# Kernel tuning notes

Hardware: AMD Instinct MI355X
Metric: run time of the kernel (lower is better)

Reference implementation:

```python
import jax, jax.numpy as jnp
import numpy as np

L, B, T, D, H = 8, 4, 1024, 1024, 16
DH = D // H
TPB, NB = 16, 64  # tokens_per_block, max_blocks; T == TPB*NB
EPS = 1e-5


def _block_causal_mask():
    idx = jnp.arange(T)
    causal = idx[:, None] >= idx[None, :]
    blk = idx // TPB
    block_diag = blk[:, None] == blk[None, :]
    return causal | block_diag  # [T, T] bool


def _ln(x, g, b):
    mu = jnp.mean(x, axis=-1, keepdims=True)
    var = jnp.mean(jnp.square(x - mu), axis=-1, keepdims=True)
    return (x - mu) * jax.lax.rsqrt(var + EPS) * g + b


def setup_inputs() -> dict:
    key = jax.random.key(0)
    ks = jax.random.split(key, 8)
    s = 0.02
    inp = {
        'sequences': jax.random.normal(ks[0], (B, T, D), jnp.float32),
        'Wq': jax.random.normal(ks[1], (L, D, D), jnp.float32) * s,
        'bq': jnp.zeros((L, D), jnp.float32),
        'Wk': jax.random.normal(ks[2], (L, D, D), jnp.float32) * s,
        'bk': jnp.zeros((L, D), jnp.float32),
        'Wv': jax.random.normal(ks[3], (L, D, D), jnp.float32) * s,
        'bv': jnp.zeros((L, D), jnp.float32),
        'Wp': jax.random.normal(ks[4], (L, D, D), jnp.float32) * s,
        'bp': jnp.zeros((L, D), jnp.float32),
        'ln1_g': jnp.ones((L, D), jnp.float32),
        'ln1_b': jnp.zeros((L, D), jnp.float32),
        'ln2_g': jnp.ones((L, D), jnp.float32),
        'ln2_b': jnp.zeros((L, D), jnp.float32),
        'W1': jax.random.normal(ks[5], (L, D, 4 * D), jnp.float32) * s,
        'b1': jnp.zeros((L, 4 * D), jnp.float32),
        'W2': jax.random.normal(ks[6], (L, 4 * D, D), jnp.float32) * s,
        'b2': jnp.zeros((L, D), jnp.float32),
        'lnf_g': jnp.ones((D,), jnp.float32),
        'lnf_b': jnp.zeros((D,), jnp.float32),
    }
    return inp


def reference(sequences, Wq, bq, Wk, bk, Wv, bv, Wp, bp,
              ln1_g, ln1_b, ln2_g, ln2_b, W1, b1, W2, b2, lnf_g, lnf_b):
    mask = _block_causal_mask()
    scale = 1.0 / np.sqrt(DH)
    x = sequences
    for i in range(L):
        h = _ln(x, ln1_g[i], ln1_b[i])
        q = (h @ Wq[i] + bq[i]).reshape(B, T, H, DH)
        k = (h @ Wk[i] + bk[i]).reshape(B, T, H, DH)
        v = (h @ Wv[i] + bv[i]).reshape(B, T, H, DH)
        att = jnp.einsum('bthd,bshd->bhts', q, k) * scale  # [B,H,T,T]
        att = jnp.where(mask, att, -jnp.inf)
        att = jax.nn.softmax(att, axis=-1)
        y = jnp.einsum('bhts,bshd->bthd', att, v).reshape(B, T, D)
        x = x + (y @ Wp[i] + bp[i])
        h2 = _ln(x, ln2_g[i], ln2_b[i])
        ff = jax.nn.gelu(h2 @ W1[i] + b1[i], approximate=False) @ W2[i] + b2[i]
        x = x + ff
    return _ln(x, lnf_g, lnf_b)
```

## Files before the change

kernel.cpp:

```cpp
#include <hip/hip_runtime.h>
#include <hip/hip_bf16.h>
#include <math.h>

#define B_ 4
#define T_ 1024
#define D_ 1024
#define H_ 16
#define DH_ 64
#define M_ 4096
#define QSTR_ 3072
#define EPS_ 1e-5f

typedef __attribute__((ext_vector_type(4))) float f32x4;
typedef __attribute__((ext_vector_type(8))) short s16x8;

#if __has_builtin(__builtin_amdgcn_exp2f)
#define EXP2F __builtin_amdgcn_exp2f
#else
#define EXP2F exp2f
#endif

__device__ __forceinline__ float gelu_f(float x) {
  return 0.5f * x * (1.0f + erff(x * 0.70710678118654752f));
}
__device__ __forceinline__ float b2f(unsigned short u) {
  union { unsigned int i; float f; } c; c.i = ((unsigned int)u) << 16; return c.f;
}
__device__ __forceinline__ unsigned short f2b(float f) {
  __hip_bfloat16 h = __float2bfloat16(f);
  return *reinterpret_cast<unsigned short*>(&h);
}
__device__ __forceinline__ void g2l16(void* l, const void* g) {
  __builtin_amdgcn_global_load_lds(
      (const __attribute__((address_space(1))) void*)g,
      (__attribute__((address_space(3))) void*)l, 16, 0, 0);
}

template<bool BF16OUT>
__global__ __launch_bounds__(256) void ln_kernel(
    const float* __restrict__ in, void* __restrict__ out,
    const float* __restrict__ g, const float* __restrict__ b) {
  const int row = blockIdx.x;
  const int tid = threadIdx.x;
  const float* rp = in + (size_t)row * D_;
  float4 v = *reinterpret_cast<const float4*>(rp + tid * 4);
  float s = v.x + v.y + v.z + v.w;
  float s2 = v.x * v.x + v.y * v.y + v.z * v.z + v.w * v.w;
#pragma unroll
  for (int off = 1; off < 64; off <<= 1) {
    s += __shfl_xor(s, off);
    s2 += __shfl_xor(s2, off);
  }
  __shared__ float red[2][4];
  const int wid = tid >> 6;
  if ((tid & 63) == 0) { red[0][wid] = s; red[1][wid] = s2; }
  __syncthreads();
  s = red[0][0] + red[0][1] + red[0][2] + red[0][3];
  s2 = red[1][0] + red[1][1] + red[1][2] + red[1][3];
  const float mu = s * (1.0f / D_);
  const float var = s2 * (1.0f / D_) - mu * mu;
  const float rs = rsqrtf(var + EPS_);
  float4 gv = *reinterpret_cast<const float4*>(g + tid * 4);
  float4 bv = *reinterpret_cast<const float4*>(b + tid * 4);
  float o0 = (v.x - mu) * rs * gv.x + bv.x;
  float o1 = (v.y - mu) * rs * gv.y + bv.y;
  float o2 = (v.z - mu) * rs * gv.z + bv.z;
  float o3 = (v.w - mu) * rs * gv.w + bv.w;
  if (BF16OUT) {
    ushort4 pk;
    pk.x = f2b(o0); pk.y = f2b(o1); pk.z = f2b(o2); pk.w = f2b(o3);
    *reinterpret_cast<ushort4*>((unsigned short*)out + (size_t)row * D_ + tid * 4) = pk;
  } else {
    *reinterpret_cast<float4*>((float*)out + (size_t)row * D_ + tid * 4) =
        make_float4(o0, o1, o2, o3);
  }
}

__global__ __launch_bounds__(256) void concat_bias(
    const float* __restrict__ bq, const float* __restrict__ bk,
    const float* __restrict__ bv, float* __restrict__ out) {
  const int i = blockIdx.x * 256 + threadIdx.x;
  const int l = i / QSTR_, c = i % QSTR_;
  const float* src = (c < 1024) ? bq : ((c < 2048) ? bk : bv);
  out[i] = src[l * 1024 + (c & 1023)];
}

__global__ __launch_bounds__(256) void reduce_add(
    float* __restrict__ x, const float* __restrict__ p) {
  const int i = blockIdx.x * 256 + threadIdx.x;
  float4 a = reinterpret_cast<float4*>(x)[i];
  float4 b = reinterpret_cast<const float4*>(p)[i];
  a.x += b.x; a.y += b.y; a.z += b.z; a.w += b.w;
  reinterpret_cast<float4*>(x)[i] = a;
}

__device__ __forceinline__ void transpose_tile(
    const float* __restrict__ src, int sld,
    __hip_bfloat16* __restrict__ dst, int dld, int k0, int n0) {
  __shared__ float tile[32][33];
  const int t = threadIdx.x;
  const int r = t >> 3;
  const int cq = (t & 7) * 4;
  float4 vv = *reinterpret_cast<const float4*>(src + (size_t)(k0 + r) * sld + n0 + cq);
  tile[r][cq + 0] = vv.x; tile[r][cq + 1] = vv.y;
  tile[r][cq + 2] = vv.z; tile[r][cq + 3] = vv.w;
  __syncthreads();
  ushort4 o;
  o.x = f2b(tile[cq + 0][r]); o.y = f2b(tile[cq + 1][r]);
  o.z = f2b(tile[cq + 2][r]); o.w = f2b(tile[cq + 3][r]);
  *reinterpret_cast<ushort4*>((unsigned short*)dst + (size_t)(n0 + r) * dld + k0 + cq) = o;
}

struct TrAll {
  const float *wq, *wk, *wv, *wp, *w1, *w2;
  __hip_bfloat16 *dqkv, *dp, *d1, *d2;
};

__global__ __launch_bounds__(256) void transpose_all(TrAll a) {
  const int t = blockIdx.x;
  const float* src;
  __hip_bfloat16* dst;
  int sld, dld, k0, n0;
  if (t < 4096) {
    const int m = t >> 10, tile = t & 1023;
    k0 = (tile >> 5) * 32; n0 = (tile & 31) * 32;
    src = (m == 0) ? a.wq : (m == 1) ? a.wk : (m == 2) ? a.wv : a.wp;
    sld = 1024; dld = 1024;
    dst = (m < 3) ? (a.dqkv + (size_t)m * 1024 * 1024) : a.dp;
  } else if (t < 8192) {
    const int tile = t - 4096;
    k0 = (tile & 31) * 32; n0 = (tile >> 5) * 32;
    src = a.w1; sld = 4096; dst = a.d1; dld = 1024;
  } else {
    const int tile = t - 8192;
    k0 = (tile >> 5) * 32; n0 = (tile & 31) * 32;
    src = a.w2; sld = 1024; dst = a.d2; dld = 4096;
  }
  transpose_tile(src, sld, dst, dld, k0, n0);
}

template<int MODE, int BN>
__global__ __launch_bounds__(256) void gemm_mfma(
    const __hip_bfloat16* __restrict__ A,
    const __hip_bfloat16* __restrict__ Bt,
    const float* __restrict__ bias,
    void* __restrict__ Cout, int N, int K) {
  __shared__ short As[3][128 * 32];
  __shared__ short Bs[3][BN * 32];
  int bid = blockIdx.y * gridDim.x + blockIdx.x;
  const int nwg = gridDim.x * gridDim.y;
  bid = (bid & 7) * (nwg >> 3) + (bid >> 3);
  const int gn = (bid % gridDim.x) * BN;
  const int gm = (bid / gridDim.x) * 128;

  const int tid = threadIdx.x;
  const int wid = tid >> 6, lane = tid & 63;
  constexpr int MR = (BN == 128) ? 4 : 2;
  const int wm = (BN == 128) ? (wid >> 1) : wid;
  const int wn = (BN == 128) ? (wid & 1) : 0;
  const int fr = lane & 15, kg = lane >> 4;

  const int ldr = lane >> 2;
  const int ldk = (((lane & 3) ^ ((lane >> 3) & 3)) * 8);
  const unsigned short* ap =
      (const unsigned short*)A + (size_t)(gm + wid * 32 + ldr) * K + ldk;
  const unsigned short* bp =
      (const unsigned short*)Bt +
      (size_t)(gn + ((BN == 128) ? wid * 32 : wid * 16) + ldr) * K + ldk;

  const int nkt = K >> 5;

#define STAGE_T(t, buf)                                                    \
  {                                                                        \
    const unsigned short* a_ = ap + (size_t)(t) * 32;                      \
    g2l16((char*)As[buf] + (wid * 2) * 1024, a_);                          \
    g2l16((char*)As[buf] + (wid * 2 + 1) * 1024, a_ + (size_t)16 * K);     \
    const unsigned short* b_ = bp + (size_t)(t) * 32;                      \
    if (BN == 128) {                                                       \
      g2l16((char*)Bs[buf] + (wid * 2) * 1024, b_);                        \
      g2l16((char*)Bs[buf] + (wid * 2 + 1) * 1024, b_ + (size_t)16 * K);   \
    } else {                                                               \
      g2l16((char*)Bs[buf] + wid * 1024, b_);                              \
    }                                                                      \
  }

  STAGE_T(0, 0);
  STAGE_T(1, 1);

  const int cxa = (kg ^ ((fr >> 1) & 3)) * 8;
  f32x4 acc[MR][4] = {};
  for (int t = 0; t < nkt; ++t) {
    const int buf = t % 3;
    if (t + 2 < nkt) STAGE_T(t + 2, (t + 2) % 3);
    const int rem = nkt - 1 - t;
    if (rem >= 2) {
      if (BN == 128) asm volatile("s_waitcnt vmcnt(8)" ::: "memory");
      else           asm volatile("s_waitcnt vmcnt(6)" ::: "memory");
    } else if (rem == 1) {
      if (BN == 128) asm volatile("s_waitcnt vmcnt(4)" ::: "memory");
      else           asm volatile("s_waitcnt vmcnt(3)" ::: "memory");
    } else {
      asm volatile("s_waitcnt vmcnt(0)" ::: "memory");
    }
    __builtin_amdgcn_s_barrier();
    __builtin_amdgcn_sched_barrier(0);
    s16x8 af[MR], bfr[4];
#pragma unroll
    for (int m = 0; m < MR; ++m)
      af[m] = *reinterpret_cast<const s16x8*>(
          &As[buf][(wm * (16 * MR) + m * 16 + fr) * 32 + cxa]);
#pragma unroll
    for (int n = 0; n < 4; ++n)
      bfr[n] = *reinterpret_cast<const s16x8*>(
          &Bs[buf][(wn * 64 + n * 16 + fr) * 32 + cxa]);
#pragma unroll
    for (int m = 0; m < MR; ++m)
#pragma unroll
      for (int n = 0; n < 4; ++n)
        acc[m][n] = __builtin_amdgcn_mfma_f32_16x16x32_bf16(af[m], bfr[n], acc[m][n], 0, 0, 0);
    __builtin_amdgcn_sched_barrier(0);
    __builtin_amdgcn_s_barrier();
  }
#undef STAGE_T

  const int r0 = gm + wm * (16 * MR);
  const int c0 = gn + wn * 64;
  float bb[4];
#pragma unroll
  for (int n = 0; n < 4; ++n)
    bb[n] = bias ? bias[c0 + n * 16 + fr] : 0.0f;
#pragma unroll
  for (int m = 0; m < MR; ++m) {
#pragma unroll
    for (int j = 0; j < 4; ++j) {
      const int row = r0 + m * 16 + kg * 4 + j;
#pragma unroll
      for (int n = 0; n < 4; ++n) {
        float val = acc[m][n][j] + bb[n];
        const size_t idx = (size_t)row * N + c0 + n * 16 + fr;
        if (MODE == 0) {
          ((unsigned short*)Cout)[idx] = f2b(val);
        } else if (MODE == 1) {
          float* cp = (float*)Cout + idx;
          *cp = *cp + val;
        } else {
          ((unsigned short*)Cout)[idx] = f2b(gelu_f(val));
        }
      }
    }
  }
}

template<int MODE>
__global__ __launch_bounds__(512) void gemm_w256(
    const __hip_bfloat16* __restrict__ A,
    const __hip_bfloat16* __restrict__ Bt,
    const float* __restrict__ bias,
    void* __restrict__ Cout, float* __restrict__ P,
    int N, int K, int KS) {
  __shared__ short As[3][128 * 32];
  __shared__ short Bs[3][256 * 32];
  int bid = blockIdx.y * gridDim.x + blockIdx.x;
  const int nwg = gridDim.x * gridDim.y;
  bid = (bid & 7) * (nwg >> 3) + (bid >> 3);
  const int gn = (bid % gridDim.x) * 256;
  const int gm = (bid / gridDim.x) * 128;
  const int koff = (MODE == 3) ? blockIdx.z * KS : 0;

  const int tid = threadIdx.x;
  const int wid = tid >> 6, lane = tid & 63;
  const int wm = wid & 1, wn = wid >> 1;
  const int fr = lane & 15, kg = lane >> 4;

  const int ldr = lane >> 2;
  const int ldk = (((lane & 3) ^ ((lane >> 3) & 3)) * 8);
  const unsigned short* ap =
      (const unsigned short*)A + (size_t)(gm + wid * 16 + ldr) * K + koff + ldk;
  const unsigned short* bp =
      (const unsigned short*)Bt + (size_t)(gn + wid * 32 + ldr) * K + koff + ldk;

  const int nkt = ((MODE == 3) ? KS : K) >> 5;

#define STAGE_W(t, buf)                                                    \
  {                                                                        \
    g2l16((char*)As[buf] + wid * 1024, ap + (size_t)(t) * 32);             \
    const unsigned short* b_ = bp + (size_t)(t) * 32;                      \
    g2l16((char*)Bs[buf] + (wid * 2) * 1024, b_);                          \
    g2l16((char*)Bs[buf] + (wid * 2 + 1) * 1024, b_ + (size_t)16 * K);     \
  }

  STAGE_W(0, 0);
  STAGE_W(1, 1);

  const int cxa = (kg ^ ((fr >> 1) & 3)) * 8;
  f32x4 acc[4][4] = {};
  for (int t = 0; t < nkt; ++t) {
    const int buf = t % 3;
    if (t + 2 < nkt) STAGE_W(t + 2, (t + 2) % 3);
    const int rem = nkt - 1 - t;
    if (rem >= 2)      asm volatile("s_waitcnt vmcnt(6)" ::: "memory");
    else if (rem == 1) asm volatile("s_waitcnt vmcnt(3)" ::: "memory");
    else               asm volatile("s_waitcnt vmcnt(0)" ::: "memory");
    __builtin_amdgcn_s_barrier();
    __builtin_amdgcn_sched_barrier(0);
    s16x8 af[4], bfr[4];
#pragma unroll
    for (int m = 0; m < 4; ++m)
      af[m] = *reinterpret_cast<const s16x8*>(
          &As[buf][(wm * 64 + m * 16 + fr) * 32 + cxa]);
#pragma unroll
    for (int n = 0; n < 4; ++n)
      bfr[n] = *reinterpret_cast<const s16x8*>(
          &Bs[buf][(wn * 64 + n * 16 + fr) * 32 + cxa]);
#pragma unroll
    for (int m = 0; m < 4; ++m)
#pragma unroll
      for (int n = 0; n < 4; ++n)
        acc[m][n] = __builtin_amdgcn_mfma_f32_16x16x32_bf16(af[m], bfr[n], acc[m][n], 0, 0, 0);
    __builtin_amdgcn_sched_barrier(0);
    __builtin_amdgcn_s_barrier();
  }
#undef STAGE_W

  const int r0 = gm + wm * 64;
  const int c0 = gn + wn * 64;
  if (MODE == 3 && blockIdx.z == 1) {
#pragma unroll
    for (int m = 0; m < 4; ++m)
#pragma unroll
      for (int j = 0; j < 4; ++j) {
        const int row = r0 + m * 16 + kg * 4 + j;
#pragma unroll
        for (int n = 0; n < 4; ++n)
          P[(size_t)row * N + c0 + n * 16 + fr] = acc[m][n][j];
      }
    return;
  }
  float bb[4];
#pragma unroll
  for (int n = 0; n < 4; ++n)
    bb[n] = bias ? bias[c0 + n * 16 + fr] : 0.0f;
#pragma unroll
  for (int m = 0; m < 4; ++m) {
#pragma unroll
    for (int j = 0; j < 4; ++j) {
      const int row = r0 + m * 16 + kg * 4 + j;
#pragma unroll
      for (int n = 0; n < 4; ++n) {
        float val = acc[m][n][j] + bb[n];
        const size_t idx = (size_t)row * N + c0 + n * 16 + fr;
        if (MODE == 0) {
          ((unsigned short*)Cout)[idx] = f2b(val);
        } else if (MODE == 1 || MODE == 3) {
          float* cp = (float*)Cout + idx;
          *cp = *cp + val;
        } else {
          ((unsigned short*)Cout)[idx] = f2b(gelu_f(val));
        }
      }
    }
  }
}

__global__ __launch_bounds__(256) void attn_mfma(
    const __hip_bfloat16* __restrict__ qkv, __hip_bfloat16* __restrict__ yg) {
  const int qb = 7 - blockIdx.x;
  const int hh = blockIdx.y;
  const int bb = blockIdx.z;
  __shared__ short Qs[128 * 64];
  __shared__ short Ks[64 * 64];
  __shared__ short Vt[64 * 64];
  const int tid = threadIdx.x;
  const int wid = tid >> 6, lane = tid & 63;
  const int fr = lane & 15, kg = lane >> 4;
  const size_t qb_base = (size_t)bb * T_ * QSTR_ + (size_t)hh * DH_;
  const unsigned short* qgp = (const unsigned short*)qkv + qb_base;
  const unsigned short* kgp = qgp + 1024;
  const unsigned short* vgp = qgp + 2048;
  const float C = 0.125f * 1.4426950408889634f;

  {
    const int r8 = lane >> 3, cp = lane & 7;
#pragma unroll
    for (int u = 0; u < 4; ++u) {
      const int row = wid * 32 + u * 8 + r8;
      const int c16 = cp ^ (row & 7);
      g2l16((char*)Qs + (wid * 32 + u * 8) * 128,
            qgp + (size_t)(qb * 128 + row) * QSTR_ + c16 * 8);
    }
  }
  asm volatile("s_waitcnt vmcnt(0)" ::: "memory");
  __syncthreads();
  s16x8 qf[2][2];
#pragma unroll
  for (int rg = 0; rg < 2; ++rg) {
    const int row = wid * 32 + rg * 16 + fr;
    const char* rp = (const char*)Qs + row * 128;
    qf[rg][0] = *reinterpret_cast<const s16x8*>(rp + (((0 + kg) ^ (row & 7)) << 4));
    qf[rg][1] = *reinterpret_cast<const s16x8*>(rp + (((4 + kg) ^ (row & 7)) << 4));
  }

  f32x4 acco[2][4] = {};
  float m_run[2][4], l_run[2][4];
#pragma unroll
  for (int rg = 0; rg < 2; ++rg)
#pragma unroll
    for (int j = 0; j < 4; ++j) { m_run[rg][j] = -INFINITY; l_run[rg][j] = 0.f; }

  const int q16hi = qb * 8 + wid * 2 + 1;
  const int ntile = 2 * qb + 2;
  for (int kt = 0; kt < ntile; ++kt) {
    __syncthreads();
    {
      const int r8 = lane >> 3, cp = lane & 7;
#pragma unroll
      for (int u = 0; u < 2; ++u) {
        const int row = wid * 16 + u * 8 + r8;
        const int c16 = cp ^ (row & 7);
        g2l16((char*)Ks + (wid * 16 + u * 8) * 128,
              kgp + (size_t)(kt * 64 + row) * QSTR_ + c16 * 8);
      }
    }
    {
      const int kv0 = tid >> 3;
      const int d0 = (tid & 7) * 8;
      const int rot = tid & 7;
#pragma unroll
      for (int u = 0; u < 2; ++u) {
        const int kv = u * 32 + kv0;
        s16x8 sv = *reinterpret_cast<const s16x8*>(
            vgp + (size_t)(kt * 64 + kv) * QSTR_ + d0);
#pragma unroll
        for (int j = 0; j < 8; ++j) {
          const int jj = (j + rot) & 7;
          const int d = d0 + jj;
          *(short*)((char*)Vt + d * 128 + ((((kv >> 3) ^ jj) & 7) << 4) + (kv & 7) * 2) = sv[jj];
        }
      }
    }
    asm volatile("s_waitcnt vmcnt(0)" ::: "memory");
    __syncthreads();

    if (kt * 4 <= q16hi) {
      f32x4 accs[2][4] = {};
#pragma unroll
      for (int n = 0; n < 4; ++n) {
        const int row = n * 16 + fr;
        const char* rp = (const char*)Ks + row * 128;
        s16x8 kf0 = *reinterpret_cast<const s16x8*>(rp + (((0 + kg) ^ (row & 7)) << 4));
        s16x8 kf1 = *reinterpret_cast<const s16x8*>(rp + (((4 + kg) ^ (row & 7)) << 4));
#pragma unroll
        for (int rg = 0; rg < 2; ++rg) {
          accs[rg][n] = __builtin_amdgcn_mfma_f32_16x16x32_bf16(qf[rg][0], kf0, accs[rg][n], 0, 0, 0);
          accs[rg][n] = __builtin_amdgcn_mfma_f32_16x16x32_bf16(qf[rg][1], kf1, accs[rg][n], 0, 0, 0);
        }
      }
#pragma unroll
      for (int rg = 0; rg < 2; ++rg) {
        const int q16 = qb * 8 + wid * 2 + rg;
        float mloc[4] = {-3.0e38f, -3.0e38f, -3.0e38f, -3.0e38f};
#pragma unroll
        for (int n = 0; n < 4; ++n)
          if (kt * 4 + n <= q16)
#pragma unroll
            for (int j = 0; j < 4; ++j) mloc[j] = fmaxf(mloc[j], accs[rg][n][j]);
#pragma unroll
        for (int off = 1; off < 16; off <<= 1)
#pragma unroll
          for (int j = 0; j < 4; ++j) mloc[j] = fmaxf(mloc[j], __shfl_xor(mloc[j], off));
        float a_[4];
#pragma unroll
        for (int j = 0; j < 4; ++j) {
          const float mn = fmaxf(m_run[rg][j], mloc[j]);
          a_[j] = EXP2F((m_run[rg][j] - mn) * C);
          m_run[rg][j] = mn;
        }
        float psum[4] = {};
#pragma unroll
        for (int n = 0; n < 4; ++n) {
          const bool dead = (kt * 4 + n > q16);
          const int c16b = n * 2 + (fr >> 3);
#pragma unroll
          for (int j = 0; j < 4; ++j) {
            float p = dead ? 0.0f : EXP2F((accs[rg][n][j] - m_run[rg][j]) * C);
            psum[j] += p;
            const int row = wid * 32 + rg * 16 + kg * 4 + j;
            *(short*)((char*)Qs + row * 128 + (((c16b ^ (row & 7)) & 7) << 4) + (fr & 7) * 2) =
                (short)f2b(p);
          }
        }
#pragma unroll
        for (int j = 0; j < 4; ++j) l_run[rg][j] = l_run[rg][j] * a_[j] + psum[j];
#pragma unroll
        for (int dt = 0; dt < 4; ++dt)
#pragma unroll
          for (int j = 0; j < 4; ++j) acco[rg][dt][j] *= a_[j];
      }
#pragma unroll
      for (int rg = 0; rg < 2; ++rg) {
        const int prow = wid * 32 + rg * 16 + fr;
        const char* pp = (const char*)Qs + prow * 128;
#pragma unroll
        for (int kk = 0; kk < 2; ++kk) {
          const s16x8 pf = *reinterpret_cast<const s16x8*>(
              pp + ((((kk * 4 + kg) ^ (prow & 7)) & 7) << 4));
#pragma unroll
          for (int dt = 0; dt < 4; ++dt) {
            const int vrow = dt * 16 + fr;
            const s16x8 vf = *reinterpret_cast<const s16x8*>(
                (const char*)Vt + vrow * 128 + ((((kk * 4 + kg) ^ (vrow & 7)) & 7) << 4));
            acco[rg][dt] = __builtin_amdgcn_mfma_f32_16x16x32_bf16(pf, vf, acco[rg][dt], 0, 0, 0);
          }
        }
      }
    }
  }

#pragma unroll
  for (int off = 1; off < 16; off <<= 1)
#pragma unroll
    for (int rg = 0; rg < 2; ++rg)
#pragma unroll
      for (int j = 0; j < 4; ++j) l_run[rg][j] += __shfl_xor(l_run[rg][j], off);
  unsigned short* yp = (unsigned short*)yg + (size_t)bb * T_ * D_ + (size_t)hh * DH_;
#pragma unroll
  for (int rg = 0; rg < 2; ++rg) {
    float inv[4];
#pragma unroll
    for (int j = 0; j < 4; ++j) inv[j] = 1.0f / l_run[rg][j];
#pragma unroll
    for (int dt = 0; dt < 4; ++dt)
#pragma unroll
      for (int j = 0; j < 4; ++j) {
        const int row = qb * 128 + wid * 32 + rg * 16 + kg * 4 + j;
        yp[(size_t)row * D_ + dt * 16 + fr] = f2b(acco[rg][dt][j] * inv[j]);
      }
  }
}

extern "C" void kernel_launch(void* const* d_in, const int* in_sizes, int n_in,
                              void* d_out, int out_size, void* d_ws, size_t ws_size,
                              hipStream_t stream) {
  (void)in_sizes; (void)n_in; (void)out_size; (void)ws_size;
  const float* seq  = (const float*)d_in[0];
  const float* Wq   = (const float*)d_in[1];
  const float* bq   = (const float*)d_in[2];
  const float* Wk   = (const float*)d_in[3];
  const float* bk   = (const float*)d_in[4];
  const float* Wv   = (const float*)d_in[5];
  const float* bv   = (const float*)d_in[6];
  const float* Wp   = (const float*)d_in[7];
  const float* bp   = (const float*)d_in[8];
  const float* ln1g = (const float*)d_in[9];
  const float* ln1b = (const float*)d_in[10];
  const float* ln2g = (const float*)d_in[11];
  const float* ln2b = (const float*)d_in[12];
  const float* W1   = (const float*)d_in[13];
  const float* b1   = (const float*)d_in[14];
  const float* W2   = (const float*)d_in[15];
  const float* b2   = (const float*)d_in[16];
  const float* lnfg = (const float*)d_in[17];
  const float* lnfb = (const float*)d_in[18];

  float* x = (float*)d_out;
  char* ws = (char*)d_ws;
  const size_t MB = 1024ull * 1024ull;
  typedef __hip_bfloat16 bf16;
  bf16*  wtqkv = (bf16*)(ws + 0 * MB);
  bf16*  wtp   = (bf16*)(ws + 6 * MB);
  bf16*  wtF1  = (bf16*)(ws + 8 * MB);
  bf16*  wtF2  = (bf16*)(ws + 16 * MB);
  bf16*  hb    = (bf16*)(ws + 24 * MB);
  bf16*  qkv   = (bf16*)(ws + 32 * MB);
  bf16*  mid   = (bf16*)(ws + 56 * MB);
  float* bqkv  = (float*)(ws + 88 * MB);
  float* part  = (float*)(ws + 32 * MB);

  hipMemcpyAsync(x, seq, (size_t)M_ * D_ * sizeof(float), hipMemcpyDeviceToDevice, stream);

  const dim3 blk(256);
  const dim3 blkw(512);
  concat_bias<<<96, blk, 0, stream>>>(bq, bk, bv, bqkv);

  for (int i = 0; i < 8; ++i) {
    const size_t wo  = (size_t)i * D_ * D_;
    const size_t vo  = (size_t)i * D_;
    const size_t w1o = (size_t)i * D_ * 4 * D_;

    ln_kernel<true><<<M_, blk, 0, stream>>>(x, hb, ln1g + vo, ln1b + vo);
    TrAll ta;
    ta.wq = Wq + wo; ta.wk = Wk + wo; ta.wv = Wv + wo; ta.wp = Wp + wo;
    ta.w1 = W1 + w1o; ta.w2 = W2 + w1o;
    ta.dqkv = wtqkv; ta.dp = wtp; ta.d1 = wtF1; ta.d2 = wtF2;
    transpose_all<<<12288, blk, 0, stream>>>(ta);
    gemm_w256<0><<<dim3(12, 32), blkw, 0, stream>>>(
        hb, wtqkv, bqkv + (size_t)i * QSTR_, qkv, nullptr, QSTR_, 1024, 0);
    attn_mfma<<<dim3(8, 16, 4), blk, 0, stream>>>(qkv, hb);
    gemm_mfma<1, 64><<<dim3(16, 32), blk, 0, stream>>>(hb, wtp, bp + vo, x, 1024, 1024);
    ln_kernel<true><<<M_, blk, 0, stream>>>(x, hb, ln2g + vo, ln2b + vo);
    gemm_w256<2><<<dim3(16, 32), blkw, 0, stream>>>(
        hb, wtF1, b1 + (size_t)i * 4096, mid, nullptr, 4096, 1024, 0);
    gemm_w256<3><<<dim3(4, 32, 2), blkw, 0, stream>>>(
        mid, wtF2, b2 + vo, x, part, 1024, 4096, 2048);
    reduce_add<<<4096, blk, 0, stream>>>(x, part);
  }
  ln_kernel<false><<<M_, blk, 0, stream>>>(x, x, lnfg, lnfb);
}
```

Measured before the change: 2.171 ms.

## Fuse split-K residual add into layernorm and double-buffer K/V in attention

Removes the separate reduce_add kernel. The split-K partial sum from the FFN2 GEMM is now added to x inside the next layer's LN1 kernel, or the final LN, which also writes the updated residual back. The attention kernel now double-buffers the K and V^T tiles in LDS, prefetching the next tile's K via global_load_lds and V into registers while the current tile is computed. The goal is to save one launch and a full pass over memory per layer, and to hide global load latency in attention, at the cost of more LDS and registers per block.

```diff
diff --git a/kernel.cpp b/kernel.cpp
--- a/kernel.cpp
+++ b/kernel.cpp
@@ -36,14 +36,20 @@
       (__attribute__((address_space(3))) void*)l, 16, 0, 0);
 }
 
-template<bool BF16OUT>
+template<bool BF16OUT, bool ADDP>
 __global__ __launch_bounds__(256) void ln_kernel(
-    const float* __restrict__ in, void* __restrict__ out,
+    float* __restrict__ xio, const float* __restrict__ part,
+    void* __restrict__ out,
     const float* __restrict__ g, const float* __restrict__ b) {
   const int row = blockIdx.x;
   const int tid = threadIdx.x;
-  const float* rp = in + (size_t)row * D_;
+  float* rp = xio + (size_t)row * D_;
   float4 v = *reinterpret_cast<const float4*>(rp + tid * 4);
+  if (ADDP) {
+    float4 pv = *reinterpret_cast<const float4*>(part + (size_t)row * D_ + tid * 4);
+    v.x += pv.x; v.y += pv.y; v.z += pv.z; v.w += pv.w;
+    *reinterpret_cast<float4*>(rp + tid * 4) = v;
+  }
   float s = v.x + v.y + v.z + v.w;
   float s2 = v.x * v.x + v.y * v.y + v.z * v.z + v.w * v.w;
 #pragma unroll
@@ -85,15 +91,6 @@
   out[i] = src[l * 1024 + (c & 1023)];
 }
 
-__global__ __launch_bounds__(256) void reduce_add(
-    float* __restrict__ x, const float* __restrict__ p) {
-  const int i = blockIdx.x * 256 + threadIdx.x;
-  float4 a = reinterpret_cast<float4*>(x)[i];
-  float4 b = reinterpret_cast<const float4*>(p)[i];
-  a.x += b.x; a.y += b.y; a.z += b.z; a.w += b.w;
-  reinterpret_cast<float4*>(x)[i] = a;
-}
-
 __device__ __forceinline__ void transpose_tile(
     const float* __restrict__ src, int sld,
     __hip_bfloat16* __restrict__ dst, int dld, int k0, int n0) {
@@ -368,8 +365,8 @@
   const int hh = blockIdx.y;
   const int bb = blockIdx.z;
   __shared__ short Qs[128 * 64];
-  __shared__ short Ks[64 * 64];
-  __shared__ short Vt[64 * 64];
+  __shared__ short Ks[2][64 * 64];
+  __shared__ short Vt[2][64 * 64];
   const int tid = threadIdx.x;
   const int wid = tid >> 6, lane = tid & 63;
   const int fr = lane & 15, kg = lane >> 4;
@@ -379,16 +376,27 @@
   const unsigned short* vgp = qgp + 2048;
   const float C = 0.125f * 1.4426950408889634f;
 
-  {
-    const int r8 = lane >> 3, cp = lane & 7;
-#pragma unroll
-    for (int u = 0; u < 4; ++u) {
-      const int row = wid * 32 + u * 8 + r8;
-      const int c16 = cp ^ (row & 7);
-      g2l16((char*)Qs + (wid * 32 + u * 8) * 128,
-            qgp + (size_t)(qb * 128 + row) * QSTR_ + c16 * 8);
-    }
-  }
+  const int r8 = lane >> 3, cp = lane & 7;
+#pragma unroll
+  for (int u = 0; u < 4; ++u) {
+    const int row = wid * 32 + u * 8 + r8;
+    const int c16 = cp ^ (row & 7);
+    g2l16((char*)Qs + (wid * 32 + u * 8) * 128,
+          qgp + (size_t)(qb * 128 + row) * QSTR_ + c16 * 8);
+  }
+#pragma unroll
+  for (int u = 0; u < 2; ++u) {
+    const int row = wid * 16 + u * 8 + r8;
+    const int c16 = cp ^ (row & 7);
+    g2l16((char*)Ks[0] + (wid * 16 + u * 8) * 128,
+          kgp + (size_t)row * QSTR_ + c16 * 8);
+  }
+  const int kv0 = tid >> 3;
+  const int d0 = (tid & 7) * 8;
+  const int rot = tid & 7;
+  s16x8 sva = *reinterpret_cast<const s16x8*>(vgp + (size_t)kv0 * QSTR_ + d0);
+  s16x8 svb = *reinterpret_cast<const s16x8*>(vgp + (size_t)(32 + kv0) * QSTR_ + d0);
+
   asm volatile("s_waitcnt vmcnt(0)" ::: "memory");
   __syncthreads();
   s16x8 qf[2][2];
@@ -410,43 +418,43 @@
   const int q16hi = qb * 8 + wid * 2 + 1;
   const int ntile = 2 * qb + 2;
   for (int kt = 0; kt < ntile; ++kt) {
+    const int buf = kt & 1;
+    asm volatile("s_waitcnt vmcnt(0)" ::: "memory");
+#pragma unroll
+    for (int j = 0; j < 8; ++j) {
+      const int jj = (j + rot) & 7;
+      const int d = d0 + jj;
+      *(short*)((char*)Vt[buf] + d * 128 + ((((kv0 >> 3) ^ jj) & 7) << 4) + (kv0 & 7) * 2) = sva[jj];
+    }
+#pragma unroll
+    for (int j = 0; j < 8; ++j) {
+      const int jj = (j + rot) & 7;
+      const int d = d0 + jj;
+      const int kv = 32 + kv0;
+      *(short*)((char*)Vt[buf] + d * 128 + ((((kv >> 3) ^ jj) & 7) << 4) + (kv & 7) * 2) = svb[jj];
+    }
     __syncthreads();
-    {
-      const int r8 = lane >> 3, cp = lane & 7;
+    if (kt + 1 < ntile) {
 #pragma unroll
       for (int u = 0; u < 2; ++u) {
         const int row = wid * 16 + u * 8 + r8;
         const int c16 = cp ^ (row & 7);
-        g2l16((char*)Ks + (wid * 16 + u * 8) * 128,
-              kgp + (size_t)(kt * 64 + row) * QSTR_ + c16 * 8);
-      }
+        g2l16((char*)Ks[buf ^ 1] + (wid * 16 + u * 8) * 128,
+              kgp + (size_t)((kt + 1) * 64 + row) * QSTR_ + c16 * 8);
+      }
+      sva = *reinterpret_cast<const s16x8*>(
+          vgp + (size_t)((kt + 1) * 64 + kv0) * QSTR_ + d0);
+      svb = *reinterpret_cast<const s16x8*>(
+          vgp + (size_t)((kt + 1) * 64 + 32 + kv0) * QSTR_ + d0);
     }
-    {
-      const int kv0 = tid >> 3;
-      const int d0 = (tid & 7) * 8;
-      const int rot = tid & 7;
-#pragma unroll
-      for (int u = 0; u < 2; ++u) {
-        const int kv = u * 32 + kv0;
-        s16x8 sv = *reinterpret_cast<const s16x8*>(
-            vgp + (size_t)(kt * 64 + kv) * QSTR_ + d0);
-#pragma unroll
-        for (int j = 0; j < 8; ++j) {
-          const int jj = (j + rot) & 7;
-          const int d = d0 + jj;
-          *(short*)((char*)Vt + d * 128 + ((((kv >> 3) ^ jj) & 7) << 4) + (kv & 7) * 2) = sv[jj];
-        }
-      }
-    }
-    asm volatile("s_waitcnt vmcnt(0)" ::: "memory");
-    __syncthreads();
+    __builtin_amdgcn_sched_barrier(0);
 
     if (kt * 4 <= q16hi) {
       f32x4 accs[2][4] = {};
 #pragma unroll
       for (int n = 0; n < 4; ++n) {
         const int row = n * 16 + fr;
-        const char* rp = (const char*)Ks + row * 128;
+        const char* rp = (const char*)Ks[buf] + row * 128;
         s16x8 kf0 = *reinterpret_cast<const s16x8*>(rp + (((0 + kg) ^ (row & 7)) << 4));
         s16x8 kf1 = *reinterpret_cast<const s16x8*>(rp + (((4 + kg) ^ (row & 7)) << 4));
 #pragma unroll
@@ -508,7 +516,7 @@
           for (int dt = 0; dt < 4; ++dt) {
             const int vrow = dt * 16 + fr;
             const s16x8 vf = *reinterpret_cast<const s16x8*>(
-                (const char*)Vt + vrow * 128 + ((((kk * 4 + kg) ^ (vrow & 7)) & 7) << 4));
+                (const char*)Vt[buf] + vrow * 128 + ((((kk * 4 + kg) ^ (vrow & 7)) & 7) << 4));
             acco[rg][dt] = __builtin_amdgcn_mfma_f32_16x16x32_bf16(pf, vf, acco[rg][dt], 0, 0, 0);
           }
         }
@@ -587,7 +595,10 @@
     const size_t vo  = (size_t)i * D_;
     const size_t w1o = (size_t)i * D_ * 4 * D_;
 
-    ln_kernel<true><<<M_, blk, 0, stream>>>(x, hb, ln1g + vo, ln1b + vo);
+    if (i == 0)
+      ln_kernel<true, false><<<M_, blk, 0, stream>>>(x, nullptr, hb, ln1g + vo, ln1b + vo);
+    else
+      ln_kernel<true, true><<<M_, blk, 0, stream>>>(x, part, hb, ln1g + vo, ln1b + vo);
     TrAll ta;
     ta.wq = Wq + wo; ta.wk = Wk + wo; ta.wv = Wv + wo; ta.wp = Wp + wo;
     ta.w1 = W1 + w1o; ta.w2 = W2 + w1o;
@@ -597,12 +608,11 @@
         hb, wtqkv, bqkv + (size_t)i * QSTR_, qkv, nullptr, QSTR_, 1024, 0);
     attn_mfma<<<dim3(8, 16, 4), blk, 0, stream>>>(qkv, hb);
     gemm_mfma<1, 64><<<dim3(16, 32), blk, 0, stream>>>(hb, wtp, bp + vo, x, 1024, 1024);
-    ln_kernel<true><<<M_, blk, 0, stream>>>(x, hb, ln2g + vo, ln2b + vo);
+    ln_kernel<true, false><<<M_, blk, 0, stream>>>(x, nullptr, hb, ln2g + vo, ln2b + vo);
     gemm_w256<2><<<dim3(16, 32), blkw, 0, stream>>>(
         hb, wtF1, b1 + (size_t)i * 4096, mid, nullptr, 4096, 1024, 0);
     gemm_w256<3><<<dim3(4, 32, 2), blkw, 0, stream>>>(
         mid, wtF2, b2 + vo, x, part, 1024, 4096, 2048);
-    reduce_add<<<4096, blk, 0, stream>>>(x, part);
-  }
-  ln_kernel<false><<<M_, blk, 0, stream>>>(x, x, lnfg, lnfb);
-}
+  }
+  ln_kernel<false, true><<<M_, blk, 0, stream>>>(x, part, x, lnfg, lnfb);
+}
```

New measurement: 2.180 ms. Within noise of the previous version (+0.4%).
